# Kernel optimization log

Measured on AMD Instinct MI355X. Metric: run time of the kernel, lower is better.

## Reference

```python
import jax, jax.numpy as jnp
import numpy as np

N, F, K, FP = 4096, 256, 8, 64  # nodes, in-feat, heads, out-feat per head
NEG_SLOPE = 0.2
MASK_FILL = -1e30  # stand-in for -inf (numerically safe under softmax/vjp)


def setup_inputs() -> dict:
    key = jax.random.key(0)
    k1, k2, k3, k4, k5 = jax.random.split(key, 5)
    x = jax.random.normal(k1, (N, F), dtype=jnp.float32)
    mask = jax.random.randint(k2, (1, N, N), 0, 2).astype(bool)
    idx = jnp.arange(N)
    mask = mask.at[0, idx, idx].set(True)  # self-loops guarantee no empty softmax rows
    W_w = jax.random.normal(k3, (K * FP, F), dtype=jnp.float32) * (1.0 / np.sqrt(F))
    W_b = jnp.zeros((K * FP,), dtype=jnp.float32)
    a_left = jax.random.normal(k4, (1, K, FP), dtype=jnp.float32) * 0.1
    a_right = jax.random.normal(k5, (1, K, FP), dtype=jnp.float32) * 0.1
    return {"x": x, "W_w": W_w, "W_b": W_b, "a_left": a_left, "a_right": a_right, "mask": mask}


def reference(x, W_w, W_b, a_left, a_right, mask):
    k, fp = a_left.shape[1], a_left.shape[2]
    # W(x): (N, K*F') -> (N, K, F')   [dropout p=0.0 -> identity]
    xe = (x @ W_w.T + W_b).reshape(-1, k, fp)
    # additive scores: h_left (K,N,1) + h_right (K,1,N) -> e (K,N,N)
    hl = jnp.einsum('nkf,kf->kn', xe, a_left[0])
    hr = jnp.einsum('nkf,kf->kn', xe, a_right[0])
    e = hl[:, :, None] + hr[:, None, :]
    e = jnp.where(e > 0, e, NEG_SLOPE * e)          # LeakyReLU(0.2)
    e = jnp.where(mask, e, MASK_FILL)               # masked_fill(~mask, -inf)
    a = jax.nn.softmax(e, axis=-1)                  # (K,N,N)
    # weighted sum of neighbor features: (K,N,N) x (N,K,F') -> (N,K,F')
    h_prime = jnp.einsum('knm,mkf->nkf', a, xe)
    h_prime = jax.nn.elu(h_prime)
    # non-final layer: elu again (as in source) then concat heads
    out = jax.nn.elu(h_prime).reshape(-1, k * fp)   # (N, K*F')
    return (out, mask)
```

## Files before the change

kernel.cpp:

```cpp
#include <hip/hip_runtime.h>
#include <hip/hip_bf16.h>

#define N_NODES 4096
#define F_IN    256
#define KH      8
#define KF      512
#define NEG_SLOPE 0.2f
#define EBIAS   4.0f

typedef _Float16 half8v __attribute__((ext_vector_type(8)));
typedef _Float16 half2v __attribute__((ext_vector_type(2)));
typedef __attribute__((ext_vector_type(4))) float floatx4;

union H8U4 { half8v v; unsigned u[4]; };

__device__ __forceinline__ unsigned short f2h(float f) {
    _Float16 h = (_Float16)f;
    unsigned short u; __builtin_memcpy(&u, &h, 2);
    return u;
}
__device__ __forceinline__ half2v asH2(unsigned u) {
    half2v h; __builtin_memcpy(&h, &u, 4);
    return h;
}
__device__ __forceinline__ unsigned asU(half2v h) {
    unsigned u; __builtin_memcpy(&u, &h, 4);
    return u;
}
__device__ __forceinline__ half8v ld8f(const float* p) {
    const float4 a = *(const float4*)p;
    const float4 b = *(const float4*)(p + 4);
    half8v h;
    h[0] = (_Float16)a.x; h[1] = (_Float16)a.y;
    h[2] = (_Float16)a.z; h[3] = (_Float16)a.w;
    h[4] = (_Float16)b.x; h[5] = (_Float16)b.y;
    h[6] = (_Float16)b.z; h[7] = (_Float16)b.w;
    return h;
}

__global__ __launch_bounds__(256) void mask_fused(
    const int* __restrict__ mask, float* __restrict__ outm,
    unsigned long long* __restrict__ bits) {
  const int tid = threadIdx.x;
  const size_t t4 = (size_t)blockIdx.x * 256 + tid;
  const int4 mv = ((const int4*)mask)[t4];
  float4 o;
  o.x = mv.x ? 1.f : 0.f; o.y = mv.y ? 1.f : 0.f;
  o.z = mv.z ? 1.f : 0.f; o.w = mv.w ? 1.f : 0.f;
  ((float4*)outm)[t4] = o;
  const unsigned nib = (mv.x ? 1u : 0u) | (mv.y ? 2u : 0u) |
                       (mv.z ? 4u : 0u) | (mv.w ? 8u : 0u);
  unsigned long long wv = (unsigned long long)nib << (4 * (tid & 15));
  wv |= __shfl_xor(wv, 1);
  wv |= __shfl_xor(wv, 2);
  wv |= __shfl_xor(wv, 4);
  wv |= __shfl_xor(wv, 8);
  if ((tid & 15) == 0) {
    const size_t e0 = t4 << 2;
    const size_t n = e0 >> 12;
    const size_t c = (e0 & 4095) >> 6;
    bits[c * N_NODES + n] = wv;
  }
}

__global__ __launch_bounds__(256) void mask_pack(
    const int* __restrict__ mask, unsigned long long* __restrict__ bits) {
  const size_t idx = (size_t)blockIdx.x * 256 + threadIdx.x;
  const unsigned long long b = __ballot(mask[idx] != 0);
  if ((threadIdx.x & 63) == 0) {
    const size_t w = idx >> 6;
    bits[(w & 63) * (size_t)N_NODES + (w >> 6)] = b;
  }
}
__global__ __launch_bounds__(256) void mask_copy(
    const int* __restrict__ mask, float* __restrict__ outm) {
  const size_t i4 = (size_t)blockIdx.x * 256 + threadIdx.x;
  const int4 mv = ((const int4*)mask)[i4];
  float4 o;
  o.x = mv.x ? 1.f : 0.f; o.y = mv.y ? 1.f : 0.f;
  o.z = mv.z ? 1.f : 0.f; o.w = mv.w ? 1.f : 0.f;
  ((float4*)outm)[i4] = o;
}

__global__ __launch_bounds__(256) void xe_gemm(
    const float* __restrict__ x,
    const float* __restrict__ Ww,
    const float* __restrict__ Wb,
    const float* __restrict__ al,
    const float* __restrict__ ar,
    unsigned short* __restrict__ xeB,
    float* __restrict__ hl,
    unsigned* __restrict__ EA,
    unsigned* __restrict__ EB,
    float* __restrict__ bmax) {
  const int tid = threadIdx.x;
  const int w = tid >> 6;
  const int lane = tid & 63;
  const int col16 = lane & 15;
  const int quad = lane >> 4;
  const int bx = blockIdx.x;
  const int k  = blockIdx.y;
  const int n0 = bx * 64;

  const int rowA = n0 + w * 16 + col16;
  const float* xp  = x  + (size_t)rowA * F_IN + quad * 8;
  const float* wwp = Ww + (size_t)(k * 64 + col16) * F_IN + quad * 8;

  floatx4 acc[4];
  #pragma unroll
  for (int ft = 0; ft < 4; ++ft) acc[ft] = (floatx4){0.f, 0.f, 0.f, 0.f};

  #pragma unroll
  for (int ks = 0; ks < 8; ++ks) {
    const half8v aF = ld8f(xp + ks * 32);
    #pragma unroll
    for (int ft = 0; ft < 4; ++ft) {
      const half8v bF = ld8f(wwp + (size_t)(ft * 16) * F_IN + ks * 32);
      acc[ft] = __builtin_amdgcn_mfma_f32_16x16x32_f16(aF, bF, acc[ft], 0, 0, 0);
    }
  }

  float pl[4] = {0.f, 0.f, 0.f, 0.f};
  float pr[4] = {0.f, 0.f, 0.f, 0.f};
  const int xoff = (w >> 1) * 512 + col16 * 32
                 + ((w & 1) * 2 + (quad >> 1)) * 8 + (quad & 1) * 4;
  #pragma unroll
  for (int ft = 0; ft < 4; ++ft) {
    const int c = k * 64 + ft * 16 + col16;
    const float wbv = Wb[c];
    const float a_l = al[c];
    const float a_r = ar[c];
    float v[4];
    ushort4 pk;
    #pragma unroll
    for (int i = 0; i < 4; ++i) {
      v[i] = acc[ft][i] + wbv;
      pl[i] = fmaf(v[i], a_l, pl[i]);
      pr[i] = fmaf(v[i], a_r, pr[i]);
    }
    pk.x = f2h(v[0]); pk.y = f2h(v[1]); pk.z = f2h(v[2]); pk.w = f2h(v[3]);
    unsigned short* tile = xeB + ((((size_t)(k * 4 + ft)) * 64 + bx) << 10);
    *(ushort4*)(tile + xoff) = pk;
  }
  #pragma unroll
  for (int o = 8; o > 0; o >>= 1) {
    #pragma unroll
    for (int i = 0; i < 4; ++i) {
      pl[i] += __shfl_xor(pl[i], o);
      pr[i] += __shfl_xor(pr[i], o);
    }
  }
  if (col16 == 0) {
    const int n = n0 + w * 16 + quad * 4;
    float4 o0 = {pl[0], pl[1], pl[2], pl[3]};
    *(float4*)(hl + k * N_NODES + n) = o0;
    unsigned short e1[4], e2[4];
    #pragma unroll
    for (int i = 0; i < 4; ++i) {
      e1[i] = f2h(__expf(pr[i] - EBIAS));
      e2[i] = f2h(__expf(NEG_SLOPE * (pr[i] - EBIAS)));
    }
    uint2 wa, wbv2;
    wa.x   = (unsigned)e1[0] | ((unsigned)e1[1] << 16);
    wa.y   = (unsigned)e1[2] | ((unsigned)e1[3] << 16);
    wbv2.x = (unsigned)e2[0] | ((unsigned)e2[1] << 16);
    wbv2.y = (unsigned)e2[2] | ((unsigned)e2[3] << 16);
    *(uint2*)(EA + k * 2048 + (n >> 1)) = wa;
    *(uint2*)(EB + k * 2048 + (n >> 1)) = wbv2;
  }
  float bm = (col16 == 0)
      ? fmaxf(fmaxf(pr[0], pr[1]), fmaxf(pr[2], pr[3])) : -1e30f;
  bm = fmaxf(bm, __shfl_xor(bm, 16));
  bm = fmaxf(bm, __shfl_xor(bm, 32));
  if (lane == 0) bmax[k * 256 + bx * 4 + w] = bm;
}

__global__ __launch_bounds__(256, 2) void gat_attn(
    const unsigned long long* __restrict__ mbitsT,
    const float* __restrict__ hl,
    const float* __restrict__ bmax,
    const unsigned* __restrict__ EA,
    const unsigned* __restrict__ EB,
    const unsigned short* __restrict__ xeB,
    float* __restrict__ out) {
  __shared__ float lds_acc[4][64][20];
  const int t = threadIdx.x;
  const int w4 = t >> 6;
  const int lane = t & 63;
  const int k  = blockIdx.x & 7;
  const int rg = blockIdx.x >> 3;
  const int n0 = rg * 32;
  const int row = lane & 15;
  const int quad = lane >> 4;
  const int q8 = quad * 8;

  const float4 bm4 = ((const float4*)bmax)[k * 64 + lane];
  float hm = fmaxf(fmaxf(bm4.x, bm4.y), fmaxf(bm4.z, bm4.w));
  #pragma unroll
  for (int o = 1; o < 64; o <<= 1) hm = fmaxf(hm, __shfl_xor(hm, o));

  const float* hlp = hl + k * N_NODES + n0 + row;
  const float hlA = hlp[0];
  const float hlB = hlp[16];
  const float sA = hlA + hm;
  const float MA = fmaxf(sA, NEG_SLOPE * sA);
  const float sB = hlB + hm;
  const float MB = fmaxf(sB, NEG_SLOPE * sB);
  const float c1Af = __expf(hlA + EBIAS - MA);
  const float c2Af = __expf(NEG_SLOPE * (hlA + EBIAS) - MA);
  const float c1Bf = __expf(hlB + EBIAS - MB);
  const float c2Bf = __expf(NEG_SLOPE * (hlB + EBIAS) - MB);
  const half2v c1A = {(_Float16)c1Af, (_Float16)c1Af};
  const half2v c2A = {(_Float16)c2Af, (_Float16)c2Af};
  const half2v c1B = {(_Float16)c1Bf, (_Float16)c1Bf};
  const half2v c2B = {(_Float16)c2Bf, (_Float16)c2Bf};

  const int c0 = w4 * 16;
  const int cEnd = c0 + 16;

  const unsigned* pEA = EA + k * 2048 + c0 * 32 + quad * 4;
  const unsigned* pEB = EB + k * 2048 + c0 * 32 + quad * 4;
  const unsigned long long* pM = mbitsT + (size_t)c0 * N_NODES + n0 + row;
  const unsigned short* pB = xeB + (((size_t)k * 4) << 16)
                           + ((size_t)c0 << 10) + row * 32 + q8;

  half8v ones;
  #pragma unroll
  for (int i = 0; i < 8; ++i) ones[i] = (_Float16)1.0f;

  floatx4 accA[4], accB[4];
  #pragma unroll
  for (int ft = 0; ft < 4; ++ft) {
    accA[ft] = (floatx4){0.f, 0.f, 0.f, 0.f};
    accB[ft] = (floatx4){0.f, 0.f, 0.f, 0.f};
  }
  floatx4 dpA = (floatx4){0.f, 0.f, 0.f, 0.f};
  floatx4 dpB = (floatx4){0.f, 0.f, 0.f, 0.f};

  uint4 pA0 = *(const uint4*)pEA;
  uint4 pA1 = *(const uint4*)(pEA + 16);
  uint4 pB0 = *(const uint4*)pEB;
  uint4 pB1 = *(const uint4*)(pEB + 16);
  unsigned long long pMvA = pM[0];
  unsigned long long pMvB = pM[16];

  for (int cc = c0; cc < cEnd; ++cc) {
    half8v b0, b1, b2, b3, b4, b5, b6, b7;
    b0 = *(const half8v*)pB;                     b1 = *(const half8v*)(pB + 512);
    b2 = *(const half8v*)(pB + (64 << 10));      b3 = *(const half8v*)(pB + (64 << 10) + 512);
    b4 = *(const half8v*)(pB + (128 << 10));     b5 = *(const half8v*)(pB + (128 << 10) + 512);
    b6 = *(const half8v*)(pB + (192 << 10));     b7 = *(const half8v*)(pB + (192 << 10) + 512);
    pB += 1024;
    const uint4 eA0 = pA0, eA1 = pA1, eB0 = pB0, eB1 = pB1;
    const unsigned long long mbA = pMvA, mbB = pMvB;
    pEA += 32; pEB += 32; pM += N_NODES;
    if (cc + 1 < cEnd) {
      pA0 = *(const uint4*)pEA;
      pA1 = *(const uint4*)(pEA + 16);
      pB0 = *(const uint4*)pEB;
      pB1 = *(const uint4*)(pEB + 16);
      pMvA = pM[0];
      pMvB = pM[16];
    }
    const unsigned ea_lo[4] = {eA0.x, eA0.y, eA0.z, eA0.w};
    const unsigned eb_lo[4] = {eB0.x, eB0.y, eB0.z, eB0.w};
    const unsigned ea_hi[4] = {eA1.x, eA1.y, eA1.z, eA1.w};
    const unsigned eb_hi[4] = {eB1.x, eB1.y, eB1.z, eB1.w};
    {
      const unsigned mlo = (unsigned)(mbA >> q8);
      const unsigned mhi = (unsigned)(mbA >> (32 + q8));
      H8U4 a0, a1;
      #pragma unroll
      for (int p = 0; p < 4; ++p) {
        const half2v w2 = __builtin_elementwise_max(c1A * asH2(ea_lo[p]),
                                                    c2A * asH2(eb_lo[p]));
        const unsigned tb = mlo >> (2 * p);
        a0.u[p] = asU(w2) & (((tb & 1u) | ((tb & 2u) << 15)) * 0xFFFFu);
      }
      #pragma unroll
      for (int p = 0; p < 4; ++p) {
        const half2v w2 = __builtin_elementwise_max(c1A * asH2(ea_hi[p]),
                                                    c2A * asH2(eb_hi[p]));
        const unsigned tb = mhi >> (2 * p);
        a1.u[p] = asU(w2) & (((tb & 1u) | ((tb & 2u) << 15)) * 0xFFFFu);
      }
      dpA = __builtin_amdgcn_mfma_f32_16x16x32_f16(a0.v, ones, dpA, 0, 0, 0);
      dpA = __builtin_amdgcn_mfma_f32_16x16x32_f16(a1.v, ones, dpA, 0, 0, 0);
      accA[0] = __builtin_amdgcn_mfma_f32_16x16x32_f16(a0.v, b0, accA[0], 0, 0, 0);
      accA[0] = __builtin_amdgcn_mfma_f32_16x16x32_f16(a1.v, b1, accA[0], 0, 0, 0);
      accA[1] = __builtin_amdgcn_mfma_f32_16x16x32_f16(a0.v, b2, accA[1], 0, 0, 0);
      accA[1] = __builtin_amdgcn_mfma_f32_16x16x32_f16(a1.v, b3, accA[1], 0, 0, 0);
      accA[2] = __builtin_amdgcn_mfma_f32_16x16x32_f16(a0.v, b4, accA[2], 0, 0, 0);
      accA[2] = __builtin_amdgcn_mfma_f32_16x16x32_f16(a1.v, b5, accA[2], 0, 0, 0);
      accA[3] = __builtin_amdgcn_mfma_f32_16x16x32_f16(a0.v, b6, accA[3], 0, 0, 0);
      accA[3] = __builtin_amdgcn_mfma_f32_16x16x32_f16(a1.v, b7, accA[3], 0, 0, 0);
    }
    {
      const unsigned mlo = (unsigned)(mbB >> q8);
      const unsigned mhi = (unsigned)(mbB >> (32 + q8));
      H8U4 a0, a1;
      #pragma unroll
      for (int p = 0; p < 4; ++p) {
        const half2v w2 = __builtin_elementwise_max(c1B * asH2(ea_lo[p]),
                                                    c2B * asH2(eb_lo[p]));
        const unsigned tb = mlo >> (2 * p);
        a0.u[p] = asU(w2) & (((tb & 1u) | ((tb & 2u) << 15)) * 0xFFFFu);
      }
      #pragma unroll
      for (int p = 0; p < 4; ++p) {
        const half2v w2 = __builtin_elementwise_max(c1B * asH2(ea_hi[p]),
                                                    c2B * asH2(eb_hi[p]));
        const unsigned tb = mhi >> (2 * p);
        a1.u[p] = asU(w2) & (((tb & 1u) | ((tb & 2u) << 15)) * 0xFFFFu);
      }
      dpB = __builtin_amdgcn_mfma_f32_16x16x32_f16(a0.v, ones, dpB, 0, 0, 0);
      dpB = __builtin_amdgcn_mfma_f32_16x16x32_f16(a1.v, ones, dpB, 0, 0, 0);
      accB[0] = __builtin_amdgcn_mfma_f32_16x16x32_f16(a0.v, b0, accB[0], 0, 0, 0);
      accB[0] = __builtin_amdgcn_mfma_f32_16x16x32_f16(a1.v, b1, accB[0], 0, 0, 0);
      accB[1] = __builtin_amdgcn_mfma_f32_16x16x32_f16(a0.v, b2, accB[1], 0, 0, 0);
      accB[1] = __builtin_amdgcn_mfma_f32_16x16x32_f16(a1.v, b3, accB[1], 0, 0, 0);
      accB[2] = __builtin_amdgcn_mfma_f32_16x16x32_f16(a0.v, b4, accB[2], 0, 0, 0);
      accB[2] = __builtin_amdgcn_mfma_f32_16x16x32_f16(a1.v, b5, accB[2], 0, 0, 0);
      accB[3] = __builtin_amdgcn_mfma_f32_16x16x32_f16(a0.v, b6, accB[3], 0, 0, 0);
      accB[3] = __builtin_amdgcn_mfma_f32_16x16x32_f16(a1.v, b7, accB[3], 0, 0, 0);
    }
  }

  #pragma unroll
  for (int i = 0; i < 16; ++i) lds_acc[w4][lane][i] = accA[i >> 2][i & 3];
  #pragma unroll
  for (int i = 0; i < 4; ++i) lds_acc[w4][lane][16 + i] = dpA[i];
  __syncthreads();
  #pragma unroll
  for (int j = 0; j < 4; ++j) {
    const int sl = 4 * w4 + j;
    float fa = 0.f, dpt = 0.f;
    #pragma unroll
    for (int w2 = 0; w2 < 4; ++w2) {
      fa  += lds_acc[w2][lane][sl];
      dpt += lds_acc[w2][lane][16 + j];
    }
    float v = fa / dpt;
    v = (v > 0.f) ? v : (__expf(v) - 1.f);
    v = (v > 0.f) ? v : (__expf(v) - 1.f);
    out[(size_t)(n0 + quad * 4 + j) * KF + k * 64 + w4 * 16 + row] = v;
  }
  __syncthreads();
  #pragma unroll
  for (int i = 0; i < 16; ++i) lds_acc[w4][lane][i] = accB[i >> 2][i & 3];
  #pragma unroll
  for (int i = 0; i < 4; ++i) lds_acc[w4][lane][16 + i] = dpB[i];
  __syncthreads();
  #pragma unroll
  for (int j = 0; j < 4; ++j) {
    const int sl = 4 * w4 + j;
    float fa = 0.f, dpt = 0.f;
    #pragma unroll
    for (int w2 = 0; w2 < 4; ++w2) {
      fa  += lds_acc[w2][lane][sl];
      dpt += lds_acc[w2][lane][16 + j];
    }
    float v = fa / dpt;
    v = (v > 0.f) ? v : (__expf(v) - 1.f);
    v = (v > 0.f) ? v : (__expf(v) - 1.f);
    out[(size_t)(n0 + 16 + quad * 4 + j) * KF + k * 64 + w4 * 16 + row] = v;
  }
}

extern "C" void kernel_launch(void* const* d_in, const int* in_sizes, int n_in,
                              void* d_out, int out_size, void* d_ws, size_t ws_size,
                              hipStream_t stream) {
  const float* x    = (const float*)d_in[0];
  const float* Ww   = (const float*)d_in[1];
  const float* Wb   = (const float*)d_in[2];
  const float* al   = (const float*)d_in[3];
  const float* ar   = (const float*)d_in[4];
  const int*   mask = (const int*)d_in[5];

  float* out      = (float*)d_out;
  float* out_mask = out + (size_t)N_NODES * KF;

  const bool use_ws = (ws_size >= (8u << 20));
  char* scratch = use_ws ? (char*)d_ws : (char*)out_mask;
  unsigned short* xeB  = (unsigned short*)scratch;
  float*          hl   = (float*)(scratch + (4u << 20));
  unsigned*       EA   = (unsigned*)(hl + KH * N_NODES);
  unsigned*       EB   = EA + KH * 2048;
  float*          bmax = (float*)(EB + KH * 2048);
  unsigned long long* mbitsT = (unsigned long long*)(scratch + (5u << 20));

  dim3 ga(N_NODES / 64, KH);
  xe_gemm<<<ga, 256, 0, stream>>>(x, Ww, Wb, al, ar, xeB, hl, EA, EB, bmax);

  if (use_ws) {
    mask_fused<<<(N_NODES * (size_t)N_NODES) / 1024, 256, 0, stream>>>(
        mask, out_mask, mbitsT);
    gat_attn<<<128 * KH, 256, 0, stream>>>(mbitsT, hl, bmax, EA, EB, xeB, out);
  } else {
    mask_pack<<<(N_NODES * (size_t)N_NODES) / 256, 256, 0, stream>>>(mask, mbitsT);
    gat_attn<<<128 * KH, 256, 0, stream>>>(mbitsT, hl, bmax, EA, EB, xeB, out);
    mask_copy<<<(N_NODES * (size_t)N_NODES) / (4 * 256), 256, 0, stream>>>(mask, out_mask);
  }
}
```

Baseline: 201.8 us.

## Merge xe GEMM and mask packing into one launch; prefetch B tiles in attention loop

The projection GEMM and the mask conversion/bit-packing kernels are combined into a single preamble launch, with block index ranges selecting the role. The two independent phases can then overlap on the GPU and one launch is dropped. Separately, the attention loop now double-buffers the xe B-fragment loads one iteration ahead, as it already did for EA/EB and the mask words. This raises register pressure in gat_attn, which may reduce occupancy under its launch bounds of 256 threads and 2 blocks.

Result: no change. 199.1 us (-1.4%).

```diff
diff --git a/kernel.cpp b/kernel.cpp
--- a/kernel.cpp
+++ b/kernel.cpp
@@ -38,11 +38,11 @@
     return h;
 }
 
-__global__ __launch_bounds__(256) void mask_fused(
+__device__ __forceinline__ void mask_body(
+    size_t bid, int tid,
     const int* __restrict__ mask, float* __restrict__ outm,
     unsigned long long* __restrict__ bits) {
-  const int tid = threadIdx.x;
-  const size_t t4 = (size_t)blockIdx.x * 256 + tid;
+  const size_t t4 = bid * 256 + tid;
   const int4 mv = ((const int4*)mask)[t4];
   float4 o;
   o.x = mv.x ? 1.f : 0.f; o.y = mv.y ? 1.f : 0.f;
@@ -63,26 +63,8 @@
   }
 }
 
-__global__ __launch_bounds__(256) void mask_pack(
-    const int* __restrict__ mask, unsigned long long* __restrict__ bits) {
-  const size_t idx = (size_t)blockIdx.x * 256 + threadIdx.x;
-  const unsigned long long b = __ballot(mask[idx] != 0);
-  if ((threadIdx.x & 63) == 0) {
-    const size_t w = idx >> 6;
-    bits[(w & 63) * (size_t)N_NODES + (w >> 6)] = b;
-  }
-}
-__global__ __launch_bounds__(256) void mask_copy(
-    const int* __restrict__ mask, float* __restrict__ outm) {
-  const size_t i4 = (size_t)blockIdx.x * 256 + threadIdx.x;
-  const int4 mv = ((const int4*)mask)[i4];
-  float4 o;
-  o.x = mv.x ? 1.f : 0.f; o.y = mv.y ? 1.f : 0.f;
-  o.z = mv.z ? 1.f : 0.f; o.w = mv.w ? 1.f : 0.f;
-  ((float4*)outm)[i4] = o;
-}
-
-__global__ __launch_bounds__(256) void xe_gemm(
+__device__ __forceinline__ void xe_body(
+    int bx, int k, int tid,
     const float* __restrict__ x,
     const float* __restrict__ Ww,
     const float* __restrict__ Wb,
@@ -93,13 +75,10 @@
     unsigned* __restrict__ EA,
     unsigned* __restrict__ EB,
     float* __restrict__ bmax) {
-  const int tid = threadIdx.x;
   const int w = tid >> 6;
   const int lane = tid & 63;
   const int col16 = lane & 15;
   const int quad = lane >> 4;
-  const int bx = blockIdx.x;
-  const int k  = blockIdx.y;
   const int n0 = bx * 64;
 
   const int rowA = n0 + w * 16 + col16;
@@ -173,6 +152,50 @@
   bm = fmaxf(bm, __shfl_xor(bm, 16));
   bm = fmaxf(bm, __shfl_xor(bm, 32));
   if (lane == 0) bmax[k * 256 + bx * 4 + w] = bm;
+}
+
+__global__ __launch_bounds__(256) void preamble(
+    const int* __restrict__ mask, float* __restrict__ outm,
+    unsigned long long* __restrict__ bits,
+    const float* __restrict__ x, const float* __restrict__ Ww,
+    const float* __restrict__ Wb, const float* __restrict__ al,
+    const float* __restrict__ ar, unsigned short* __restrict__ xeB,
+    float* __restrict__ hl, unsigned* __restrict__ EA,
+    unsigned* __restrict__ EB, float* __restrict__ bmax) {
+  if (blockIdx.x < 512) {
+    xe_body((int)(blockIdx.x & 63), (int)(blockIdx.x >> 6), threadIdx.x,
+            x, Ww, Wb, al, ar, xeB, hl, EA, EB, bmax);
+  } else {
+    mask_body((size_t)blockIdx.x - 512, threadIdx.x, mask, outm, bits);
+  }
+}
+
+__global__ __launch_bounds__(256) void xe_gemm_k(
+    const float* __restrict__ x, const float* __restrict__ Ww,
+    const float* __restrict__ Wb, const float* __restrict__ al,
+    const float* __restrict__ ar, unsigned short* __restrict__ xeB,
+    float* __restrict__ hl, unsigned* __restrict__ EA,
+    unsigned* __restrict__ EB, float* __restrict__ bmax) {
+  xe_body(blockIdx.x, blockIdx.y, threadIdx.x,
+          x, Ww, Wb, al, ar, xeB, hl, EA, EB, bmax);
+}
+__global__ __launch_bounds__(256) void mask_pack(
+    const int* __restrict__ mask, unsigned long long* __restrict__ bits) {
+  const size_t idx = (size_t)blockIdx.x * 256 + threadIdx.x;
+  const unsigned long long b = __ballot(mask[idx] != 0);
+  if ((threadIdx.x & 63) == 0) {
+    const size_t w = idx >> 6;
+    bits[(w & 63) * (size_t)N_NODES + (w >> 6)] = b;
+  }
+}
+__global__ __launch_bounds__(256) void mask_copy(
+    const int* __restrict__ mask, float* __restrict__ outm) {
+  const size_t i4 = (size_t)blockIdx.x * 256 + threadIdx.x;
+  const int4 mv = ((const int4*)mask)[i4];
+  float4 o;
+  o.x = mv.x ? 1.f : 0.f; o.y = mv.y ? 1.f : 0.f;
+  o.z = mv.z ? 1.f : 0.f; o.w = mv.w ? 1.f : 0.f;
+  ((float4*)outm)[i4] = o;
 }
 
 __global__ __launch_bounds__(256, 2) void gat_attn(
@@ -237,6 +260,12 @@
   floatx4 dpA = (floatx4){0.f, 0.f, 0.f, 0.f};
   floatx4 dpB = (floatx4){0.f, 0.f, 0.f, 0.f};
 
+  half8v nb0, nb1, nb2, nb3, nb4, nb5, nb6, nb7;
+  nb0 = *(const half8v*)pB;                     nb1 = *(const half8v*)(pB + 512);
+  nb2 = *(const half8v*)(pB + (64 << 10));      nb3 = *(const half8v*)(pB + (64 << 10) + 512);
+  nb4 = *(const half8v*)(pB + (128 << 10));     nb5 = *(const half8v*)(pB + (128 << 10) + 512);
+  nb6 = *(const half8v*)(pB + (192 << 10));     nb7 = *(const half8v*)(pB + (192 << 10) + 512);
+  pB += 1024;
   uint4 pA0 = *(const uint4*)pEA;
   uint4 pA1 = *(const uint4*)(pEA + 16);
   uint4 pB0 = *(const uint4*)pEB;
@@ -245,16 +274,17 @@
   unsigned long long pMvB = pM[16];
 
   for (int cc = c0; cc < cEnd; ++cc) {
-    half8v b0, b1, b2, b3, b4, b5, b6, b7;
-    b0 = *(const half8v*)pB;                     b1 = *(const half8v*)(pB + 512);
-    b2 = *(const half8v*)(pB + (64 << 10));      b3 = *(const half8v*)(pB + (64 << 10) + 512);
-    b4 = *(const half8v*)(pB + (128 << 10));     b5 = *(const half8v*)(pB + (128 << 10) + 512);
-    b6 = *(const half8v*)(pB + (192 << 10));     b7 = *(const half8v*)(pB + (192 << 10) + 512);
-    pB += 1024;
+    const half8v b0 = nb0, b1 = nb1, b2 = nb2, b3 = nb3;
+    const half8v b4 = nb4, b5 = nb5, b6 = nb6, b7 = nb7;
     const uint4 eA0 = pA0, eA1 = pA1, eB0 = pB0, eB1 = pB1;
     const unsigned long long mbA = pMvA, mbB = pMvB;
     pEA += 32; pEB += 32; pM += N_NODES;
     if (cc + 1 < cEnd) {
+      nb0 = *(const half8v*)pB;                     nb1 = *(const half8v*)(pB + 512);
+      nb2 = *(const half8v*)(pB + (64 << 10));      nb3 = *(const half8v*)(pB + (64 << 10) + 512);
+      nb4 = *(const half8v*)(pB + (128 << 10));     nb5 = *(const half8v*)(pB + (128 << 10) + 512);
+      nb6 = *(const half8v*)(pB + (192 << 10));     nb7 = *(const half8v*)(pB + (192 << 10) + 512);
+      pB += 1024;
       pA0 = *(const uint4*)pEA;
       pA1 = *(const uint4*)(pEA + 16);
       pB0 = *(const uint4*)pEB;
@@ -389,14 +419,13 @@
   float*          bmax = (float*)(EB + KH * 2048);
   unsigned long long* mbitsT = (unsigned long long*)(scratch + (5u << 20));
 
-  dim3 ga(N_NODES / 64, KH);
-  xe_gemm<<<ga, 256, 0, stream>>>(x, Ww, Wb, al, ar, xeB, hl, EA, EB, bmax);
-
   if (use_ws) {
-    mask_fused<<<(N_NODES * (size_t)N_NODES) / 1024, 256, 0, stream>>>(
-        mask, out_mask, mbitsT);
+    preamble<<<512 + (N_NODES * (size_t)N_NODES) / 1024, 256, 0, stream>>>(
+        mask, out_mask, mbitsT, x, Ww, Wb, al, ar, xeB, hl, EA, EB, bmax);
     gat_attn<<<128 * KH, 256, 0, stream>>>(mbitsT, hl, bmax, EA, EB, xeB, out);
   } else {
+    dim3 ga(N_NODES / 64, KH);
+    xe_gemm_k<<<ga, 256, 0, stream>>>(x, Ww, Wb, al, ar, xeB, hl, EA, EB, bmax);
     mask_pack<<<(N_NODES * (size_t)N_NODES) / 256, 256, 0, stream>>>(mask, mbitsT);
     gat_attn<<<128 * KH, 256, 0, stream>>>(mbitsT, hl, bmax, EA, EB, xeB, out);
     mask_copy<<<(N_NODES * (size_t)N_NODES) / (4 * 256), 256, 0, stream>>>(mask, out_mask);
```
